# Kernel tuning notes

Hardware: AMD Instinct MI355X
Metric: run time of the kernel (lower is better)

The kernel has to match this reference:

```python
import jax, jax.numpy as jnp
import numpy as np

B, S, D_IN, D_EMB, H = 2, 2048, 1024, 1024, 16
HD = D_EMB // H

def setup_inputs() -> dict:
    key = jax.random.key(0)
    k1, k2, k3 = jax.random.split(key, 3)
    # xavier-uniform style scales
    lim_qkv = float(np.sqrt(6.0 / (D_IN + 3 * D_EMB)))
    lim_o = float(np.sqrt(6.0 / (D_EMB + D_EMB)))
    return {
        "x": jax.random.normal(k1, (B, S, D_IN), dtype=jnp.float32),
        "W_qkv": jax.random.uniform(k2, (3 * D_EMB, D_IN), minval=-lim_qkv, maxval=lim_qkv, dtype=jnp.float32),
        "b_qkv": jnp.zeros((3 * D_EMB,), dtype=jnp.float32),
        "W_o": jax.random.uniform(k3, (D_EMB, D_EMB), minval=-lim_o, maxval=lim_o, dtype=jnp.float32),
        "b_o": jnp.zeros((D_EMB,), dtype=jnp.float32),
    }

def reference(x, W_qkv, b_qkv, W_o, b_o):
    b, s, _ = x.shape
    qkv = x @ W_qkv.T + b_qkv                     # [B,S,3E]
    qkv = qkv.reshape(b, s, H, 3 * HD).transpose(0, 2, 1, 3)  # [B,H,S,3*HD]
    q, k, v = jnp.split(qkv, 3, axis=-1)          # each [B,H,S,HD]
    scale = 1.0 / np.sqrt(HD)
    attn = jax.nn.softmax(jnp.einsum('bhqd,bhkd->bhqk', q, k) * scale, axis=-1)
    vals = jnp.einsum('bhqk,bhkd->bhqd', attn, v) # [B,H,S,HD]
    vals = vals.transpose(0, 2, 1, 3).reshape(b, s, D_EMB)
    return vals @ W_o.T + b_o
```

## Files before the change

kernel.cpp:

```cpp
#include <hip/hip_runtime.h>
#include <hip/hip_bf16.h>

typedef unsigned short u16;
typedef unsigned int u32;
typedef __bf16 bf16x8 __attribute__((ext_vector_type(8)));
typedef float f32x4 __attribute__((ext_vector_type(4)));
typedef u32 u32x4 __attribute__((ext_vector_type(4)));

#define MFMA16(a, b, c) __builtin_amdgcn_mfma_f32_16x16x32_bf16((a), (b), (c), 0, 0, 0)

static __device__ __forceinline__ u16 f2bf(float f) {
  __hip_bfloat16 h = __float2bfloat16(f);
  return __builtin_bit_cast(u16, h);
}

static __device__ __forceinline__ u32 pack2(float a, float b) {
  return (u32)f2bf(a) | ((u32)f2bf(b) << 16);
}

static __device__ __forceinline__ bf16x8 ldbf8(const void* p) {
  return *reinterpret_cast<const bf16x8*>(p);
}

static __device__ __forceinline__ void gload_lds16(const void* g, void* l) {
  __builtin_amdgcn_global_load_lds(
      (const __attribute__((address_space(1))) u32*)g,
      (__attribute__((address_space(3))) u32*)l, 16, 0, 0);
}

__global__ void cvt_all(const float* __restrict__ x, const float* __restrict__ wq,
                        const float* __restrict__ wo, u16* __restrict__ xb,
                        u16* __restrict__ wqb, u16* __restrict__ wob) {
  int i = blockIdx.x * 256 + threadIdx.x;
  const float* s;
  u16* d;
  int j;
  if (i < 524288) {
    s = x; d = xb; j = i;
  } else if (i < 917504) {
    s = wq; d = wqb; j = i - 524288;
  } else {
    s = wo; d = wob; j = i - 917504;
  }
  const float4* p = reinterpret_cast<const float4*>(s) + (size_t)j * 2;
  float4 a = p[0], b = p[1];
  uint4 o;
  o.x = (u32)f2bf(a.x) | ((u32)f2bf(a.y) << 16);
  o.y = (u32)f2bf(a.z) | ((u32)f2bf(a.w) << 16);
  o.z = (u32)f2bf(b.x) | ((u32)f2bf(b.y) << 16);
  o.w = (u32)f2bf(b.z) | ((u32)f2bf(b.w) << 16);
  reinterpret_cast<uint4*>(d)[j] = o;
}

template <bool BF16OUT>
__global__ __launch_bounds__(256, 3) void gemm_bt(const u16* __restrict__ A,
                                                  const u16* __restrict__ Bm,
                                                  const float* __restrict__ bias,
                                                  void* __restrict__ Cp,
                                                  int M, int N, int K) {
  __shared__ __align__(16) char As[128 * 64 * 2];
  __shared__ __align__(16) char Bs[128 * 64 * 2];
  const int tid = threadIdx.x;
  const int lane = tid & 63;
  const int wid = tid >> 6;
  const int fr = lane & 15, fg = lane >> 4;
  const int gx = gridDim.x, nwg = gx * gridDim.y;
  const int id = blockIdx.y * gx + blockIdx.x;
  const int nid = (id & 7) * (nwg >> 3) + (id >> 3);
  const int bm = nid / gx, bn = nid % gx;
  const int wm = (wid >> 1) * 64, wn = (wid & 1) * 64;

  f32x4 acc[4][4];
#pragma unroll
  for (int i = 0; i < 4; ++i)
#pragma unroll
    for (int j = 0; j < 4; ++j) acc[i][j] = (f32x4){0.f, 0.f, 0.f, 0.f};

  const int nk = K >> 6;
  for (int kt = 0; kt < nk; ++kt) {
#pragma unroll
    for (int it = 0; it < 4; ++it) {
      int q = it * 256 + tid;
      int row = q >> 3;
      int c = (q & 7) ^ (row & 7);
      gload_lds16(A + (size_t)(bm * 128 + row) * K + kt * 64 + c * 8, As + q * 16);
      gload_lds16(Bm + (size_t)(bn * 128 + row) * K + kt * 64 + c * 8, Bs + q * 16);
    }
    __syncthreads();
#pragma unroll
    for (int mk = 0; mk < 2; ++mk) {
      bf16x8 af[4], bfr[4];
#pragma unroll
      for (int i = 0; i < 4; ++i) {
        int row = wm + i * 16 + fr;
        af[i] = ldbf8(As + ((row * 128 + mk * 64 + fg * 16) ^ ((row & 7) << 4)));
      }
#pragma unroll
      for (int j = 0; j < 4; ++j) {
        int row = wn + j * 16 + fr;
        bfr[j] = ldbf8(Bs + ((row * 128 + mk * 64 + fg * 16) ^ ((row & 7) << 4)));
      }
#pragma unroll
      for (int i = 0; i < 4; ++i)
#pragma unroll
        for (int j = 0; j < 4; ++j) acc[i][j] = MFMA16(af[i], bfr[j], acc[i][j]);
    }
    __syncthreads();
  }

#pragma unroll
  for (int j = 0; j < 4; ++j) {
    int col = bn * 128 + wn + j * 16 + fr;
    float bv = bias[col];
#pragma unroll
    for (int i = 0; i < 4; ++i) {
#pragma unroll
      for (int r = 0; r < 4; ++r) {
        int row = bm * 128 + wm + i * 16 + fg * 4 + r;
        float v = acc[i][j][r] + bv;
        if (BF16OUT)
          ((u16*)Cp)[(size_t)row * N + col] = f2bf(v);
        else
          ((float*)Cp)[(size_t)row * N + col] = v;
      }
    }
  }
}

__global__ __launch_bounds__(256, 2) void attn_fwd(const u16* __restrict__ qkv,
                                                   u16* __restrict__ aout) {
  const int id = blockIdx.y * gridDim.x + blockIdx.x;
  const int xcd = id & 7, slot = id >> 3;
  const int bh = xcd * 4 + (slot >> 4);
  const int qt = slot & 15;
  const int b = bh >> 4, h = bh & 15;
  const int tid = threadIdx.x, lane = tid & 63, wid = tid >> 6;
  const int fr = lane & 15, fg = (lane >> 4) & 3;

  __shared__ __align__(16) char Ks[2][2][64 * 128];
  __shared__ __align__(16) char VTs[2][2][64 * 128];

  const int q0 = qt * 128 + wid * 32;
  const size_t bS = (size_t)b * 2048;
  const u16* kbase = qkv + bS * 3072 + h * 192 + 64;
  const u16* vbase = qkv + bS * 3072 + h * 192 + 128;

  const int krow0 = tid >> 3, krow1 = 32 + (tid >> 3);
  const int kcol = (tid & 7) * 8;
  int kw0 = (krow0 * 128 + (tid & 7) * 16) ^ ((krow0 & 7) << 4);
  int kw1 = (krow1 * 128 + (tid & 7) * 16) ^ ((krow1 & 7) << 4);
  asm volatile("" : "+v"(kw0), "+v"(kw1));
  const int vs2 = (tid >> 3) * 2;
  const int vdc = (tid & 7) * 8;
  const int vm_ = vs2 >> 5, vG = (vs2 >> 2) & 3;
  const int vu = ((vs2 >> 4) & 1) * 2 + ((vs2 >> 1) & 1);
  const int vl0 = vm_ * 32 + ((vG ^ vu) << 3) + vu * 2;
  int wof[8];
#pragma unroll
  for (int j = 0; j < 8; ++j) {
    int d = vdc + j;
    wof[j] = ((d * 128 + vl0 * 2) ^ ((((d & 7) ^ ((d >> 3) & 7))) << 4));
    asm volatile("" : "+v"(wof[j]));
  }
  int kro[2];
#pragma unroll
  for (int mk = 0; mk < 2; ++mk) {
    kro[mk] = ((fr * 128 + mk * 64 + fg * 16) ^ ((fr & 7) << 4));
    asm volatile("" : "+v"(kro[mk]));
  }
  int vadr[4][2];
#pragma unroll
  for (int tp = 0; tp < 4; ++tp)
#pragma unroll
    for (int mk = 0; mk < 2; ++mk) {
      int d = tp * 16 + fr;
      int swz = (((d & 7) ^ ((d >> 3) & 7)) << 4);
      vadr[tp][mk] = ((d * 128 + mk * 64 + fg * 16) ^ swz);
      asm volatile("" : "+v"(vadr[tp][mk]));
    }

  bf16x8 qf[2][2];
#pragma unroll
  for (int qs = 0; qs < 2; ++qs)
#pragma unroll
    for (int mk = 0; mk < 2; ++mk) {
      bf16x8 v =
          ldbf8(qkv + (bS + q0 + qs * 16 + fr) * 3072 + h * 192 + mk * 32 + fg * 8);
#pragma unroll
      for (int e = 0; e < 8; ++e) v[e] = (__bf16)((float)v[e] * 0.1803368801f);
      qf[qs][mk] = v;
    }

  const u32 one2 = 0x3F803F80u;
  const u32x4 onev = {one2, one2, one2, one2};
  const bf16x8 onesf = __builtin_bit_cast(bf16x8, onev);
  float zs = 0.f;
  asm volatile("" : "+v"(zs));
  const f32x4 zacc = {zs, zs, zs, zs};

  f32x4 oacc0[4], oacc1[4];
#pragma unroll
  for (int t = 0; t < 4; ++t) {
    oacc0[t] = (f32x4){0.f, 0.f, 0.f, 0.f};
    oacc1[t] = (f32x4){0.f, 0.f, 0.f, 0.f};
  }
  f32x4 lacc0 = (f32x4){0.f, 0.f, 0.f, 0.f};
  f32x4 lacc1 = (f32x4){0.f, 0.f, 0.f, 0.f};

#define LOADT(S0, K0, K1, K2, K3, V0, V1, V2, V3)                                         \
  K0 = *reinterpret_cast<const uint4*>(kbase + (size_t)((S0) + krow0) * 3072 + kcol);      \
  K1 = *reinterpret_cast<const uint4*>(kbase + (size_t)((S0) + krow1) * 3072 + kcol);      \
  K2 = *reinterpret_cast<const uint4*>(kbase + (size_t)((S0) + 64 + krow0) * 3072 + kcol); \
  K3 = *reinterpret_cast<const uint4*>(kbase + (size_t)((S0) + 64 + krow1) * 3072 + kcol); \
  V0 = *reinterpret_cast<const uint4*>(vbase + (size_t)((S0) + vs2) * 3072 + vdc);         \
  V1 = *reinterpret_cast<const uint4*>(vbase + (size_t)((S0) + vs2 + 1) * 3072 + vdc);     \
  V2 = *reinterpret_cast<const uint4*>(vbase + (size_t)((S0) + 64 + vs2) * 3072 + vdc);    \
  V3 = *reinterpret_cast<const uint4*>(vbase + (size_t)((S0) + 64 + vs2 + 1) * 3072 + vdc);

#define STAGEV1(VTP, V0, V1)                           \
  {                                                    \
    const u16* e0 = reinterpret_cast<const u16*>(&V0); \
    const u16* e1 = reinterpret_cast<const u16*>(&V1); \
    _Pragma("unroll") for (int j = 0; j < 8; ++j) {    \
      u32 w = (u32)e0[j] | ((u32)e1[j] << 16);         \
      *reinterpret_cast<u32*>((VTP) + wof[j]) = w;     \
    }                                                  \
  }

#define STAGE(BUF, K0, K1, K2, K3, V0, V1, V2, V3)        \
  {                                                       \
    *reinterpret_cast<uint4*>(Ks[BUF][0] + kw0) = K0;     \
    *reinterpret_cast<uint4*>(Ks[BUF][0] + kw1) = K1;     \
    *reinterpret_cast<uint4*>(Ks[BUF][1] + kw0) = K2;     \
    *reinterpret_cast<uint4*>(Ks[BUF][1] + kw1) = K3;     \
    STAGEV1(VTs[BUF][0], V0, V1);                         \
    STAGEV1(VTs[BUF][1], V2, V3);                         \
  }

#define BAR()                                          \
  {                                                    \
    __builtin_amdgcn_sched_barrier(0);                 \
    asm volatile("s_waitcnt lgkmcnt(0)" ::: "memory"); \
    __builtin_amdgcn_s_barrier();                      \
    __builtin_amdgcn_sched_barrier(0);                 \
  }

#define COMPUTE1(KSP, VTP)                                                     \
  {                                                                            \
    f32x4 sc0[4], sc1[4];                                                      \
    __builtin_amdgcn_s_setprio(1);                                             \
    _Pragma("unroll") for (int t = 0; t < 4; ++t) {                            \
      bf16x8 kf0 = ldbf8((KSP) + kro[0] + t * 2048);                           \
      bf16x8 kf1 = ldbf8((KSP) + kro[1] + t * 2048);                           \
      sc0[t] = MFMA16(kf0, qf[0][0], zacc);                                    \
      sc0[t] = MFMA16(kf1, qf[0][1], sc0[t]);                                  \
      sc1[t] = MFMA16(kf0, qf[1][0], zacc);                                    \
      sc1[t] = MFMA16(kf1, qf[1][1], sc1[t]);                                  \
    }                                                                          \
    __builtin_amdgcn_s_setprio(0);                                             \
    u32 Wp0[2][4], Wp1[2][4];                                                  \
    _Pragma("unroll") for (int t = 0; t < 4; ++t) {                            \
      Wp0[0][t] = pack2(__builtin_amdgcn_exp2f(sc0[t][0]),                     \
                        __builtin_amdgcn_exp2f(sc0[t][1]));                    \
      Wp0[1][t] = pack2(__builtin_amdgcn_exp2f(sc0[t][2]),                     \
                        __builtin_amdgcn_exp2f(sc0[t][3]));                    \
      Wp1[0][t] = pack2(__builtin_amdgcn_exp2f(sc1[t][0]),                     \
                        __builtin_amdgcn_exp2f(sc1[t][1]));                    \
      Wp1[1][t] = pack2(__builtin_amdgcn_exp2f(sc1[t][2]),                     \
                        __builtin_amdgcn_exp2f(sc1[t][3]));                    \
    }                                                                          \
    _Pragma("unroll") for (int mk = 0; mk < 2; ++mk) {                         \
      u32x4 pk0, pk1;                                                          \
      pk0.x = Wp0[0][2 * mk];                                                  \
      pk0.y = (u32)__shfl_xor((int)Wp0[1][2 * mk], 16);                        \
      pk0.z = (u32)__shfl_xor((int)Wp0[0][2 * mk + 1], 32);                    \
      pk0.w = (u32)__shfl_xor((int)Wp0[1][2 * mk + 1], 48);                    \
      pk1.x = Wp1[0][2 * mk];                                                  \
      pk1.y = (u32)__shfl_xor((int)Wp1[1][2 * mk], 16);                        \
      pk1.z = (u32)__shfl_xor((int)Wp1[0][2 * mk + 1], 32);                    \
      pk1.w = (u32)__shfl_xor((int)Wp1[1][2 * mk + 1], 48);                    \
      bf16x8 pa0 = __builtin_bit_cast(bf16x8, pk0);                            \
      bf16x8 pa1 = __builtin_bit_cast(bf16x8, pk1);                            \
      __builtin_amdgcn_s_setprio(1);                                           \
      lacc0 = MFMA16(pa0, onesf, lacc0);                                       \
      lacc1 = MFMA16(pa1, onesf, lacc1);                                       \
      _Pragma("unroll") for (int tp = 0; tp < 4; ++tp) {                       \
        bf16x8 vf = ldbf8((VTP) + vadr[tp][mk]);                               \
        oacc0[tp] = MFMA16(pa0, vf, oacc0[tp]);                                \
        oacc1[tp] = MFMA16(pa1, vf, oacc1[tp]);                                \
      }                                                                        \
      __builtin_amdgcn_s_setprio(0);                                           \
    }                                                                          \
  }

#define COMPUTE(BUF)                   \
  {                                    \
    COMPUTE1(Ks[BUF][0], VTs[BUF][0]); \
    COMPUTE1(Ks[BUF][1], VTs[BUF][1]); \
  }

  uint4 ka0, ka1, ka2, ka3, va0, va1, va2, va3;
  uint4 kb0, kb1, kb2, kb3, vb0, vb1, vb2, vb3;
  LOADT(0, ka0, ka1, ka2, ka3, va0, va1, va2, va3);
  STAGE(0, ka0, ka1, ka2, ka3, va0, va1, va2, va3);
  LOADT(128, kb0, kb1, kb2, kb3, vb0, vb1, vb2, vb3);
  BAR();
  for (int kv = 0; kv < 16; kv += 2) {
    {
      int s0n = (kv + 2 < 16) ? (kv + 2) * 128 : 0;
      LOADT(s0n, ka0, ka1, ka2, ka3, va0, va1, va2, va3);
    }
    STAGE(1, kb0, kb1, kb2, kb3, vb0, vb1, vb2, vb3);
    COMPUTE(0);
    BAR();
    {
      int s0n = (kv + 3 < 16) ? (kv + 3) * 128 : 128;
      LOADT(s0n, kb0, kb1, kb2, kb3, vb0, vb1, vb2, vb3);
    }
    STAGE(0, ka0, ka1, ka2, ka3, va0, va1, va2, va3);
    COMPUTE(1);
    BAR();
  }
#undef LOADT
#undef STAGEV1
#undef STAGE
#undef BAR
#undef COMPUTE1
#undef COMPUTE

  {
    float invb0[4], invb1[4];
#pragma unroll
    for (int r = 0; r < 4; ++r) {
      invb0[r] = 1.f / lacc0[r];
      invb1[r] = 1.f / lacc1[r];
    }
#pragma unroll
    for (int tp = 0; tp < 4; ++tp) {
#pragma unroll
      for (int r = 0; r < 4; ++r) {
        int row0 = q0 + fg * 4 + r;
        aout[(bS + row0) * 1024 + h * 64 + tp * 16 + fr] =
            f2bf(oacc0[tp][r] * invb0[r]);
        int row1 = q0 + 16 + fg * 4 + r;
        aout[(bS + row1) * 1024 + h * 64 + tp * 16 + fr] =
            f2bf(oacc1[tp][r] * invb1[r]);
      }
    }
  }
}

extern "C" void kernel_launch(void* const* d_in, const int* in_sizes, int n_in,
                              void* d_out, int out_size, void* d_ws, size_t ws_size,
                              hipStream_t stream) {
  const float* x = (const float*)d_in[0];
  const float* Wqkv = (const float*)d_in[1];
  const float* bqkv = (const float*)d_in[2];
  const float* Wo = (const float*)d_in[3];
  const float* bo = (const float*)d_in[4];
  float* out = (float*)d_out;
  char* ws = (char*)d_ws;

  u16* xb = (u16*)(ws);
  u16* wqb = (u16*)(ws + 8388608);
  u16* wob = (u16*)(ws + 14680064);
  u16* qkvb = (u16*)(ws + 16777216);
  u16* attb = (u16*)(ws + 41943040);

  cvt_all<<<4096, 256, 0, stream>>>(x, Wqkv, Wo, xb, wqb, wob);

  gemm_bt<true><<<dim3(24, 32), 256, 0, stream>>>(xb, wqb, bqkv, qkvb, 4096, 3072, 1024);
  attn_fwd<<<dim3(16, 32), 256, 0, stream>>>(qkvb, attb);
  gemm_bt<false><<<dim3(8, 32), 256, 0, stream>>>(attb, wob, bo, out, 4096, 1024, 1024);
}
```

Baseline: 108.9 us.

## Double attention query tile per block to reuse K/V tiles across more rows

Each attention block now handles 256 query rows (64 per wave) instead of 128, so every K/V tile loaded into LDS feeds twice as many MFMAs. The grid is halved to 256 blocks and launch bounds drop to one block per SM to make room for the larger accumulator and score register arrays. This reduces global K/V traffic and LDS staging per unit of work, but lowers occupancy and leaves only 256 blocks for the device's CUs, which risks underfilling the GPU and raising register pressure.

```diff
diff --git a/kernel.cpp b/kernel.cpp
--- a/kernel.cpp
+++ b/kernel.cpp
@@ -127,12 +127,12 @@
   }
 }
 
-__global__ __launch_bounds__(256, 2) void attn_fwd(const u16* __restrict__ qkv,
+__global__ __launch_bounds__(256, 1) void attn_fwd(const u16* __restrict__ qkv,
                                                    u16* __restrict__ aout) {
   const int id = blockIdx.y * gridDim.x + blockIdx.x;
   const int xcd = id & 7, slot = id >> 3;
-  const int bh = xcd * 4 + (slot >> 4);
-  const int qt = slot & 15;
+  const int bh = xcd * 4 + (slot >> 3);
+  const int qt = slot & 7;
   const int b = bh >> 4, h = bh & 15;
   const int tid = threadIdx.x, lane = tid & 63, wid = tid >> 6;
   const int fr = lane & 15, fg = (lane >> 4) & 3;
@@ -140,7 +140,7 @@
   __shared__ __align__(16) char Ks[2][2][64 * 128];
   __shared__ __align__(16) char VTs[2][2][64 * 128];
 
-  const int q0 = qt * 128 + wid * 32;
+  const int q0 = qt * 256 + wid * 64;
   const size_t bS = (size_t)b * 2048;
   const u16* kbase = qkv + bS * 3072 + h * 192 + 64;
   const u16* vbase = qkv + bS * 3072 + h * 192 + 128;
@@ -179,9 +179,9 @@
       asm volatile("" : "+v"(vadr[tp][mk]));
     }
 
-  bf16x8 qf[2][2];
-#pragma unroll
-  for (int qs = 0; qs < 2; ++qs)
+  bf16x8 qf[4][2];
+#pragma unroll
+  for (int qs = 0; qs < 4; ++qs)
 #pragma unroll
     for (int mk = 0; mk < 2; ++mk) {
       bf16x8 v =
@@ -198,14 +198,14 @@
   asm volatile("" : "+v"(zs));
   const f32x4 zacc = {zs, zs, zs, zs};
 
-  f32x4 oacc0[4], oacc1[4];
-#pragma unroll
-  for (int t = 0; t < 4; ++t) {
-    oacc0[t] = (f32x4){0.f, 0.f, 0.f, 0.f};
-    oacc1[t] = (f32x4){0.f, 0.f, 0.f, 0.f};
-  }
-  f32x4 lacc0 = (f32x4){0.f, 0.f, 0.f, 0.f};
-  f32x4 lacc1 = (f32x4){0.f, 0.f, 0.f, 0.f};
+  f32x4 oacc[4][4];
+  f32x4 lacc[4];
+#pragma unroll
+  for (int qs = 0; qs < 4; ++qs) {
+#pragma unroll
+    for (int t = 0; t < 4; ++t) oacc[qs][t] = (f32x4){0.f, 0.f, 0.f, 0.f};
+    lacc[qs] = (f32x4){0.f, 0.f, 0.f, 0.f};
+  }
 
 #define LOADT(S0, K0, K1, K2, K3, V0, V1, V2, V3)                                         \
   K0 = *reinterpret_cast<const uint4*>(kbase + (size_t)((S0) + krow0) * 3072 + kcol);      \
@@ -247,47 +247,42 @@
 
 #define COMPUTE1(KSP, VTP)                                                     \
   {                                                                            \
-    f32x4 sc0[4], sc1[4];                                                      \
+    f32x4 sc[4][4];                                                            \
     __builtin_amdgcn_s_setprio(1);                                             \
     _Pragma("unroll") for (int t = 0; t < 4; ++t) {                            \
       bf16x8 kf0 = ldbf8((KSP) + kro[0] + t * 2048);                           \
       bf16x8 kf1 = ldbf8((KSP) + kro[1] + t * 2048);                           \
-      sc0[t] = MFMA16(kf0, qf[0][0], zacc);                                    \
-      sc0[t] = MFMA16(kf1, qf[0][1], sc0[t]);                                  \
-      sc1[t] = MFMA16(kf0, qf[1][0], zacc);                                    \
-      sc1[t] = MFMA16(kf1, qf[1][1], sc1[t]);                                  \
+      _Pragma("unroll") for (int qs = 0; qs < 4; ++qs) {                       \
+        sc[qs][t] = MFMA16(kf0, qf[qs][0], zacc);                              \
+        sc[qs][t] = MFMA16(kf1, qf[qs][1], sc[qs][t]);                         \
+      }                                                                        \
     }                                                                          \
     __builtin_amdgcn_s_setprio(0);                                             \
-    u32 Wp0[2][4], Wp1[2][4];                                                  \
-    _Pragma("unroll") for (int t = 0; t < 4; ++t) {                            \
-      Wp0[0][t] = pack2(__builtin_amdgcn_exp2f(sc0[t][0]),                     \
-                        __builtin_amdgcn_exp2f(sc0[t][1]));                    \
-      Wp0[1][t] = pack2(__builtin_amdgcn_exp2f(sc0[t][2]),                     \
-                        __builtin_amdgcn_exp2f(sc0[t][3]));                    \
-      Wp1[0][t] = pack2(__builtin_amdgcn_exp2f(sc1[t][0]),                     \
-                        __builtin_amdgcn_exp2f(sc1[t][1]));                    \
-      Wp1[1][t] = pack2(__builtin_amdgcn_exp2f(sc1[t][2]),                     \
-                        __builtin_amdgcn_exp2f(sc1[t][3]));                    \
+    u32 Wp[4][2][4];                                                           \
+    _Pragma("unroll") for (int qs = 0; qs < 4; ++qs)                           \
+        _Pragma("unroll") for (int t = 0; t < 4; ++t) {                        \
+      Wp[qs][0][t] = pack2(__builtin_amdgcn_exp2f(sc[qs][t][0]),               \
+                           __builtin_amdgcn_exp2f(sc[qs][t][1]));              \
+      Wp[qs][1][t] = pack2(__builtin_amdgcn_exp2f(sc[qs][t][2]),               \
+                           __builtin_amdgcn_exp2f(sc[qs][t][3]));              \
     }                                                                          \
     _Pragma("unroll") for (int mk = 0; mk < 2; ++mk) {                         \
-      u32x4 pk0, pk1;                                                          \
-      pk0.x = Wp0[0][2 * mk];                                                  \
-      pk0.y = (u32)__shfl_xor((int)Wp0[1][2 * mk], 16);                        \
-      pk0.z = (u32)__shfl_xor((int)Wp0[0][2 * mk + 1], 32);                    \
-      pk0.w = (u32)__shfl_xor((int)Wp0[1][2 * mk + 1], 48);                    \
-      pk1.x = Wp1[0][2 * mk];                                                  \
-      pk1.y = (u32)__shfl_xor((int)Wp1[1][2 * mk], 16);                        \
-      pk1.z = (u32)__shfl_xor((int)Wp1[0][2 * mk + 1], 32);                    \
-      pk1.w = (u32)__shfl_xor((int)Wp1[1][2 * mk + 1], 48);                    \
-      bf16x8 pa0 = __builtin_bit_cast(bf16x8, pk0);                            \
-      bf16x8 pa1 = __builtin_bit_cast(bf16x8, pk1);                            \
+      bf16x8 pa[4];                                                            \
+      _Pragma("unroll") for (int qs = 0; qs < 4; ++qs) {                       \
+        u32x4 pk;                                                              \
+        pk.x = Wp[qs][0][2 * mk];                                              \
+        pk.y = (u32)__shfl_xor((int)Wp[qs][1][2 * mk], 16);                    \
+        pk.z = (u32)__shfl_xor((int)Wp[qs][0][2 * mk + 1], 32);                \
+        pk.w = (u32)__shfl_xor((int)Wp[qs][1][2 * mk + 1], 48);                \
+        pa[qs] = __builtin_bit_cast(bf16x8, pk);                               \
+      }                                                                        \
       __builtin_amdgcn_s_setprio(1);                                           \
-      lacc0 = MFMA16(pa0, onesf, lacc0);                                       \
-      lacc1 = MFMA16(pa1, onesf, lacc1);                                       \
+      _Pragma("unroll") for (int qs = 0; qs < 4; ++qs) lacc[qs] =              \
+          MFMA16(pa[qs], onesf, lacc[qs]);                                     \
       _Pragma("unroll") for (int tp = 0; tp < 4; ++tp) {                       \
         bf16x8 vf = ldbf8((VTP) + vadr[tp][mk]);                               \
-        oacc0[tp] = MFMA16(pa0, vf, oacc0[tp]);                                \
-        oacc1[tp] = MFMA16(pa1, vf, oacc1[tp]);                                \
+        _Pragma("unroll") for (int qs = 0; qs < 4; ++qs) oacc[qs][tp] =        \
+            MFMA16(pa[qs], vf, oacc[qs][tp]);                                  \
       }                                                                        \
       __builtin_amdgcn_s_setprio(0);                                           \
     }                                                                          \
@@ -328,23 +323,18 @@
 #undef COMPUTE1
 #undef COMPUTE
 
-  {
-    float invb0[4], invb1[4];
-#pragma unroll
-    for (int r = 0; r < 4; ++r) {
-      invb0[r] = 1.f / lacc0[r];
-      invb1[r] = 1.f / lacc1[r];
-    }
+#pragma unroll
+  for (int qs = 0; qs < 4; ++qs) {
+    float invb[4];
+#pragma unroll
+    for (int r = 0; r < 4; ++r) invb[r] = 1.f / lacc[qs][r];
 #pragma unroll
     for (int tp = 0; tp < 4; ++tp) {
 #pragma unroll
       for (int r = 0; r < 4; ++r) {
-        int row0 = q0 + fg * 4 + r;
-        aout[(bS + row0) * 1024 + h * 64 + tp * 16 + fr] =
-            f2bf(oacc0[tp][r] * invb0[r]);
-        int row1 = q0 + 16 + fg * 4 + r;
-        aout[(bS + row1) * 1024 + h * 64 + tp * 16 + fr] =
-            f2bf(oacc1[tp][r] * invb1[r]);
+        int row = q0 + qs * 16 + fg * 4 + r;
+        aout[(bS + row) * 1024 + h * 64 + tp * 16 + fr] =
+            f2bf(oacc[qs][tp][r] * invb[r]);
       }
     }
   }
@@ -370,6 +360,6 @@
   cvt_all<<<4096, 256, 0, stream>>>(x, Wqkv, Wo, xb, wqb, wob);
 
   gemm_bt<true><<<dim3(24, 32), 256, 0, stream>>>(xb, wqb, bqkv, qkvb, 4096, 3072, 1024);
-  attn_fwd<<<dim3(16, 32), 256, 0, stream>>>(qkvb, attb);
+  attn_fwd<<<dim3(8, 32), 256, 0, stream>>>(qkvb, attb);
   gemm_bt<false><<<dim3(8, 32), 256, 0, stream>>>(attb, wob, bo, out, 4096, 1024, 1024);
 }
```

Measured after the change: 115.5 us. 1.06x slower.
